# Optimization experiments

Hardware: AMD Instinct MI355X
Metric: run time of the kernel (lower is better)

The kernel has to match this reference:

```python
import jax, jax.numpy as jnp
import numpy as np

TGT, BSZ, E = 256, 8, 256
SRC = 4096
H = 8
HD = E // H


def setup_inputs() -> dict:
    key = jax.random.key(0)
    ks = jax.random.split(key, 6)
    return {
        "query": jax.random.normal(ks[0], (TGT, BSZ, E), dtype=jnp.float32),
        "key": jax.random.normal(ks[1], (SRC, BSZ, E), dtype=jnp.float32),
        "value": jax.random.normal(ks[2], (SRC, BSZ, E), dtype=jnp.float32),
        "proposal_mask": jax.random.uniform(ks[3], (BSZ, TGT, SRC), dtype=jnp.float32),
        "out_proj_weight": jax.random.normal(ks[4], (E, E), dtype=jnp.float32) * (1.0 / np.sqrt(E)),
        "out_proj_bias": jax.random.normal(ks[5], (E,), dtype=jnp.float32) * 0.01,
    }


def reference(query, key, value, proposal_mask, out_proj_weight, out_proj_bias):
    tgt_len, bsz, embed_dim = query.shape
    src_len = key.shape[0]
    num_heads = H
    head_dim = embed_dim // num_heads

    # v: (src, bsz, E) -> (src, bsz*H, hd) -> (bsz*H, src, hd); index q = b*H + h
    v = value.reshape(src_len, bsz * num_heads, head_dim).transpose(1, 0, 2)

    # proposal_mask (bsz, tgt, src); torch loop+stack produces mask_nhead[b*H+h] = proposal_mask[b]
    mask_nhead = jnp.repeat(proposal_mask, num_heads, axis=0)  # (bsz*H, tgt, src)

    # weighted sum of values per head (no score compute)
    attn_output = jnp.einsum('qts,qsc->qtc', mask_nhead, v)  # (bsz*H, tgt, hd)

    # (bsz*H, tgt, hd) -> (tgt, bsz*H, hd) -> (tgt, bsz, E)
    attn_output = attn_output.transpose(1, 0, 2).reshape(tgt_len, bsz, embed_dim)

    # out projection (outDecoderLayer=False)
    attn_output = attn_output @ out_proj_weight.T + out_proj_bias

    # averaged weights: mask repeated per head -> mean over heads == proposal_mask
    attn_weights = mask_nhead.reshape(bsz, num_heads, tgt_len, src_len).sum(axis=1) / num_heads
    return attn_output, attn_weights
```

## Files before the change

### kernel.cpp

```cpp
#include <hip/hip_runtime.h>
#include <hip/hip_bf16.h>

#define TGT 256
#define BSZ 8
#define E   256
#define SRC 4096

typedef __attribute__((ext_vector_type(8))) short           bf16x8;
typedef __attribute__((ext_vector_type(4))) float           f32x4;
typedef __attribute__((ext_vector_type(4))) float           f4;
typedef __attribute__((ext_vector_type(8))) unsigned short  u16x8;
typedef __attribute__((ext_vector_type(4))) unsigned short  u16x4;

__device__ inline unsigned short f2b(float x) {
    union { __hip_bfloat16 h; unsigned short u; } cv;
    cv.h = __float2bfloat16(x);
    return cv.u;
}

__device__ inline bf16x8 cvt8v(const float* __restrict__ p) {
    f4 lo = *(const f4*)p;
    f4 hi = *(const f4*)(p + 4);
    bf16x8 r;
    #pragma unroll
    for (int j = 0; j < 4; ++j) { r[j] = (short)f2b(lo[j]); r[4 + j] = (short)f2b(hi[j]); }
    return r;
}

__global__ __launch_bounds__(128) void prep_w(
    const float* __restrict__ wgt, unsigned short* __restrict__ wf)
{
    int o    = blockIdx.x * 128 + threadIdx.x;
    int et   = o >> 9;
    int ks   = (o >> 6) & 7;
    int lane = o & 63;
    int quad = lane >> 4, l15 = lane & 15;
    bf16x8 v = cvt8v(wgt + (size_t)(et * 16 + l15) * E + ks * 32 + quad * 8);
    *(bf16x8*)&wf[(size_t)o * 8] = v;
}

__global__ __launch_bounds__(512, 4) void prep_vw(
    const float* __restrict__ value, const unsigned short* __restrict__ wf,
    const float* __restrict__ bias,
    unsigned short* __restrict__ vwf, float* __restrict__ out0)
{
    const int tid = threadIdx.x;

    if (blockIdx.y == 8) {
        #pragma unroll
        for (int s = 0; s < 4; ++s) {
            int f4i = s * 32768 + blockIdx.x * 512 + tid;
            *(f4*)(out0 + (size_t)f4i * 4) = *(const f4*)(bias + (f4i & 63) * 4);
        }
        return;
    }

    __shared__ unsigned short tile[64 * 264];
    const int sc64 = blockIdx.x;
    const int b    = blockIdx.y;
    const int s0   = sc64 * 64;

    #pragma unroll
    for (int i = 0; i < 8; ++i) {
        int lin = i * 512 + tid;
        int row = lin >> 6;
        int c4  = lin & 63;
        f4 v = *(const f4*)(value + (size_t)(s0 + row) * (BSZ * E)
                                  + (size_t)b * E + c4 * 4);
        u16x4 pk;
        #pragma unroll
        for (int j = 0; j < 4; ++j) pk[j] = f2b(v[j]);
        *(u16x4*)&tile[row * 264 + c4 * 4] = pk;
    }
    __syncthreads();

    const int w    = tid >> 6;
    const int lane = tid & 63;
    const int quad = lane >> 4;
    const int l15  = lane & 15;
    const int mt   = w >> 1;
    const int et0  = (w & 1) * 8;

    bf16x8 a[8];
    #pragma unroll
    for (int ks = 0; ks < 8; ++ks)
        a[ks] = *(const bf16x8*)&tile[(mt * 16 + l15) * 264 + ks * 32 + quad * 8];
    __syncthreads();

    const unsigned short* bfw = wf + ((size_t)et0 * 8) * 512 + (size_t)lane * 8;
    f32x4 acc[8] = {};
    #pragma unroll
    for (int ks = 0; ks < 8; ++ks) {
        bf16x8 bb[8];
        #pragma unroll
        for (int e = 0; e < 8; ++e)
            bb[e] = *(const bf16x8*)(bfw + (size_t)(e * 8 + ks) * 512);
        #pragma unroll
        for (int e = 0; e < 8; ++e)
            acc[e] = __builtin_amdgcn_mfma_f32_16x16x32_bf16(a[ks], bb[e], acc[e], 0, 0, 0);
    }

    #pragma unroll
    for (int e = 0; e < 8; ++e)
        #pragma unroll
        for (int r = 0; r < 4; ++r)
            tile[(mt * 16 + quad * 4 + r) * 264 + (et0 + e) * 16 + l15] = f2b(acc[e][r]);
    __syncthreads();

    #pragma unroll
    for (int i = 0; i < 4; ++i) {
        int o    = i * 512 + tid;
        int et   = o >> 7;
        int ksl  = (o >> 6) & 1;
        int ln   = o & 63;
        int q2   = ln >> 4, p15 = ln & 15;
        u16x8 pk;
        #pragma unroll
        for (int j = 0; j < 8; ++j)
            pk[j] = tile[(ksl * 32 + q2 * 8 + j) * 264 + et * 16 + p15];
        size_t ks = (size_t)sc64 * 2 + ksl;
        *(u16x8*)&vwf[((((size_t)b * 16 + et) * 128 + ks) * 64 + ln) * 8] = pk;
    }
}

#define GP 520

__global__ __launch_bounds__(512, 4) void gemm1(
    const float* __restrict__ mask,
    const unsigned short* __restrict__ vwf,
    float* __restrict__ out1,
    float* __restrict__ out0)
{
    __shared__ unsigned short As[32 * GP];
    const int bx  = blockIdx.x;
    const int b   = bx & 7;
    const int tt  = (bx >> 3) & 7;
    const int kc  = bx >> 6;
    const int t0  = tt * 32;
    const int k0  = kc * 512;
    const int tid = threadIdx.x;
    const int w    = tid >> 6;
    const int lane = tid & 63;
    const int quad = lane >> 4;
    const int l15  = lane & 15;

    const float* mbase = mask + (size_t)b * TGT * SRC + (size_t)t0 * SRC + k0;
    float*       obase = out1 + (size_t)b * TGT * SRC + (size_t)t0 * SRC + k0;

    const int srow = tid >> 4;
    const int sc4  = tid & 15;
    f4 mv[8];
    #pragma unroll
    for (int j = 0; j < 8; ++j)
        mv[j] = *(const f4*)(mbase + (size_t)srow * SRC + (sc4 + j * 16) * 4);
    #pragma unroll
    for (int j = 0; j < 8; ++j) {
        u16x4 pk;
        #pragma unroll
        for (int t = 0; t < 4; ++t) pk[t] = f2b(mv[j][t]);
        *(u16x4*)&As[srow * GP + (sc4 + j * 16) * 4] = pk;
    }
    __syncthreads();

    #pragma unroll
    for (int j = 0; j < 8; ++j)
        *(f4*)(obase + (size_t)srow * SRC + (sc4 + j * 16) * 4) = mv[j];

    const unsigned short* bfr0 = vwf + (((size_t)b * 16 + 2 * w) * 128 + (size_t)kc * 16) * 512;
    const unsigned short* bfr1 = bfr0 + (size_t)128 * 512;

    f32x4 acc00 = {}, acc01 = {}, acc10 = {}, acc11 = {};
    #pragma unroll 4
    for (int q = 0; q < 16; ++q) {
        bf16x8 B0 = *(const bf16x8*)(bfr0 + ((size_t)q * 64 + lane) * 8);
        bf16x8 B1 = *(const bf16x8*)(bfr1 + ((size_t)q * 64 + lane) * 8);
        bf16x8 a0 = *(const bf16x8*)&As[ l15       * GP + q * 32 + quad * 8];
        bf16x8 a1 = *(const bf16x8*)&As[(l15 + 16) * GP + q * 32 + quad * 8];
        acc00 = __builtin_amdgcn_mfma_f32_16x16x32_bf16(a0, B0, acc00, 0, 0, 0);
        acc01 = __builtin_amdgcn_mfma_f32_16x16x32_bf16(a0, B1, acc01, 0, 0, 0);
        acc10 = __builtin_amdgcn_mfma_f32_16x16x32_bf16(a1, B0, acc10, 0, 0, 0);
        acc11 = __builtin_amdgcn_mfma_f32_16x16x32_bf16(a1, B1, acc11, 0, 0, 0);
    }

    {
        const int c0 = w * 32 + l15;
        #pragma unroll
        for (int r = 0; r < 4; ++r) {
            int tA = t0 + quad * 4 + r;
            int tB = tA + 16;
            float* oA = out0 + (size_t)tA * (BSZ * E) + (size_t)b * E;
            float* oB = out0 + (size_t)tB * (BSZ * E) + (size_t)b * E;
            atomicAdd(oA + c0,      acc00[r]);
            atomicAdd(oA + c0 + 16, acc01[r]);
            atomicAdd(oB + c0,      acc10[r]);
            atomicAdd(oB + c0 + 16, acc11[r]);
        }
    }
}

extern "C" void kernel_launch(void* const* d_in, const int* in_sizes, int n_in,
                              void* d_out, int out_size, void* d_ws, size_t ws_size,
                              hipStream_t stream)
{
    const float* value = (const float*)d_in[2];
    const float* mask  = (const float*)d_in[3];
    const float* wgt   = (const float*)d_in[4];
    const float* bias  = (const float*)d_in[5];

    float* out0 = (float*)d_out;
    float* out1 = (float*)d_out + (size_t)TGT * BSZ * E;

    unsigned short* vwf = (unsigned short*)d_ws;
    unsigned short* wf  = vwf + (size_t)BSZ * E * SRC;

    prep_w <<<64, 128, 0, stream>>>(wgt, wf);
    prep_vw<<<dim3(64, 9), 512, 0, stream>>>(value, wf, bias, vwf, out0);
    gemm1  <<<512, 512, 0, stream>>>(mask, vwf, out1, out0);
}
```

Measured before the change: 160.9 us.

## Halve tile sizes, write V·W fragments directly, use nontemporal mask streaming

Both prep_vw and gemm1 now run twice as many blocks of 256 threads over 32-row and 16-row tiles. prep_vw stores the MFMA accumulators straight into the B-fragment layout of vwf, which drops the shared-memory transpose stage and two barriers. gemm1 reads the mask and copies it to the weights output with nontemporal loads and stores so the streaming traffic does not pollute cache. Each gemm1 wave now computes four 16-column tiles against one A row block, so every vwf fragment is fetched by twice as many blocks.

```diff
diff --git a/kernel.cpp b/kernel.cpp
--- a/kernel.cpp
+++ b/kernel.cpp
@@ -39,7 +39,7 @@
     *(bf16x8*)&wf[(size_t)o * 8] = v;
 }
 
-__global__ __launch_bounds__(512, 4) void prep_vw(
+__global__ __launch_bounds__(256, 4) void prep_vw(
     const float* __restrict__ value, const unsigned short* __restrict__ wf,
     const float* __restrict__ bias,
     unsigned short* __restrict__ vwf, float* __restrict__ out0)
@@ -49,20 +49,20 @@
     if (blockIdx.y == 8) {
         #pragma unroll
         for (int s = 0; s < 4; ++s) {
-            int f4i = s * 32768 + blockIdx.x * 512 + tid;
+            int f4i = s * 32768 + blockIdx.x * 256 + tid;
             *(f4*)(out0 + (size_t)f4i * 4) = *(const f4*)(bias + (f4i & 63) * 4);
         }
         return;
     }
 
-    __shared__ unsigned short tile[64 * 264];
-    const int sc64 = blockIdx.x;
+    __shared__ unsigned short tile[32 * 264];
+    const int sc32 = blockIdx.x;
     const int b    = blockIdx.y;
-    const int s0   = sc64 * 64;
+    const int s0   = sc32 * 32;
 
     #pragma unroll
     for (int i = 0; i < 8; ++i) {
-        int lin = i * 512 + tid;
+        int lin = i * 256 + tid;
         int row = lin >> 6;
         int c4  = lin & 63;
         f4 v = *(const f4*)(value + (size_t)(s0 + row) * (BSZ * E)
@@ -85,7 +85,6 @@
     #pragma unroll
     for (int ks = 0; ks < 8; ++ks)
         a[ks] = *(const bf16x8*)&tile[(mt * 16 + l15) * 264 + ks * 32 + quad * 8];
-    __syncthreads();
 
     const unsigned short* bfw = wf + ((size_t)et0 * 8) * 512 + (size_t)lane * 8;
     f32x4 acc[8] = {};
@@ -100,43 +99,31 @@
             acc[e] = __builtin_amdgcn_mfma_f32_16x16x32_bf16(a[ks], bb[e], acc[e], 0, 0, 0);
     }
 
-    #pragma unroll
-    for (int e = 0; e < 8; ++e)
-        #pragma unroll
-        for (int r = 0; r < 4; ++r)
-            tile[(mt * 16 + quad * 4 + r) * 264 + (et0 + e) * 16 + l15] = f2b(acc[e][r]);
-    __syncthreads();
-
-    #pragma unroll
-    for (int i = 0; i < 4; ++i) {
-        int o    = i * 512 + tid;
-        int et   = o >> 7;
-        int ksl  = (o >> 6) & 1;
-        int ln   = o & 63;
-        int q2   = ln >> 4, p15 = ln & 15;
-        u16x8 pk;
-        #pragma unroll
-        for (int j = 0; j < 8; ++j)
-            pk[j] = tile[(ksl * 32 + q2 * 8 + j) * 264 + et * 16 + p15];
-        size_t ks = (size_t)sc64 * 2 + ksl;
-        *(u16x8*)&vwf[((((size_t)b * 16 + et) * 128 + ks) * 64 + ln) * 8] = pk;
+    const int lp = (mt * 2 + (quad >> 1)) * 16 + l15;
+    const int j0 = (quad & 1) * 4;
+    #pragma unroll
+    for (int e = 0; e < 8; ++e) {
+        u16x4 pk;
+        #pragma unroll
+        for (int r = 0; r < 4; ++r) pk[r] = f2b(acc[e][r]);
+        *(u16x4*)&vwf[((((size_t)b * 16 + et0 + e) * 128 + sc32) * 64 + lp) * 8 + j0] = pk;
     }
 }
 
 #define GP 520
 
-__global__ __launch_bounds__(512, 4) void gemm1(
+__global__ __launch_bounds__(256, 4) void gemm1(
     const float* __restrict__ mask,
     const unsigned short* __restrict__ vwf,
     float* __restrict__ out1,
     float* __restrict__ out0)
 {
-    __shared__ unsigned short As[32 * GP];
+    __shared__ unsigned short As[16 * GP];
     const int bx  = blockIdx.x;
     const int b   = bx & 7;
-    const int tt  = (bx >> 3) & 7;
-    const int kc  = bx >> 6;
-    const int t0  = tt * 32;
+    const int tt  = (bx >> 3) & 15;
+    const int kc  = bx >> 7;
+    const int t0  = tt * 16;
     const int k0  = kc * 512;
     const int tid = threadIdx.x;
     const int w    = tid >> 6;
@@ -152,7 +139,8 @@
     f4 mv[8];
     #pragma unroll
     for (int j = 0; j < 8; ++j)
-        mv[j] = *(const f4*)(mbase + (size_t)srow * SRC + (sc4 + j * 16) * 4);
+        mv[j] = __builtin_nontemporal_load(
+                    (const f4*)(mbase + (size_t)srow * SRC + (sc4 + j * 16) * 4));
     #pragma unroll
     for (int j = 0; j < 8; ++j) {
         u16x4 pk;
@@ -164,36 +152,33 @@
 
     #pragma unroll
     for (int j = 0; j < 8; ++j)
-        *(f4*)(obase + (size_t)srow * SRC + (sc4 + j * 16) * 4) = mv[j];
-
-    const unsigned short* bfr0 = vwf + (((size_t)b * 16 + 2 * w) * 128 + (size_t)kc * 16) * 512;
-    const unsigned short* bfr1 = bfr0 + (size_t)128 * 512;
-
-    f32x4 acc00 = {}, acc01 = {}, acc10 = {}, acc11 = {};
+        __builtin_nontemporal_store(
+            mv[j], (f4*)(obase + (size_t)srow * SRC + (sc4 + j * 16) * 4));
+
+    const unsigned short* bfr = vwf + (((size_t)b * 16 + (size_t)w * 4) * 128
+                                       + (size_t)kc * 16) * 512 + (size_t)lane * 8;
+
+    f32x4 acc[4] = {};
     #pragma unroll 4
     for (int q = 0; q < 16; ++q) {
-        bf16x8 B0 = *(const bf16x8*)(bfr0 + ((size_t)q * 64 + lane) * 8);
-        bf16x8 B1 = *(const bf16x8*)(bfr1 + ((size_t)q * 64 + lane) * 8);
-        bf16x8 a0 = *(const bf16x8*)&As[ l15       * GP + q * 32 + quad * 8];
-        bf16x8 a1 = *(const bf16x8*)&As[(l15 + 16) * GP + q * 32 + quad * 8];
-        acc00 = __builtin_amdgcn_mfma_f32_16x16x32_bf16(a0, B0, acc00, 0, 0, 0);
-        acc01 = __builtin_amdgcn_mfma_f32_16x16x32_bf16(a0, B1, acc01, 0, 0, 0);
-        acc10 = __builtin_amdgcn_mfma_f32_16x16x32_bf16(a1, B0, acc10, 0, 0, 0);
-        acc11 = __builtin_amdgcn_mfma_f32_16x16x32_bf16(a1, B1, acc11, 0, 0, 0);
-    }
-
-    {
-        const int c0 = w * 32 + l15;
+        bf16x8 a0 = *(const bf16x8*)&As[l15 * GP + q * 32 + quad * 8];
+        bf16x8 B0 = *(const bf16x8*)(bfr + ((size_t)0 * 128 + q) * 512);
+        bf16x8 B1 = *(const bf16x8*)(bfr + ((size_t)1 * 128 + q) * 512);
+        bf16x8 B2 = *(const bf16x8*)(bfr + ((size_t)2 * 128 + q) * 512);
+        bf16x8 B3 = *(const bf16x8*)(bfr + ((size_t)3 * 128 + q) * 512);
+        acc[0] = __builtin_amdgcn_mfma_f32_16x16x32_bf16(a0, B0, acc[0], 0, 0, 0);
+        acc[1] = __builtin_amdgcn_mfma_f32_16x16x32_bf16(a0, B1, acc[1], 0, 0, 0);
+        acc[2] = __builtin_amdgcn_mfma_f32_16x16x32_bf16(a0, B2, acc[2], 0, 0, 0);
+        acc[3] = __builtin_amdgcn_mfma_f32_16x16x32_bf16(a0, B3, acc[3], 0, 0, 0);
+    }
+
+    #pragma unroll
+    for (int e = 0; e < 4; ++e) {
+        int ecol = (w * 4 + e) * 16 + l15;
         #pragma unroll
         for (int r = 0; r < 4; ++r) {
-            int tA = t0 + quad * 4 + r;
-            int tB = tA + 16;
-            float* oA = out0 + (size_t)tA * (BSZ * E) + (size_t)b * E;
-            float* oB = out0 + (size_t)tB * (BSZ * E) + (size_t)b * E;
-            atomicAdd(oA + c0,      acc00[r]);
-            atomicAdd(oA + c0 + 16, acc01[r]);
-            atomicAdd(oB + c0,      acc10[r]);
-            atomicAdd(oB + c0 + 16, acc11[r]);
+            int t = t0 + quad * 4 + r;
+            atomicAdd(out0 + (size_t)t * (BSZ * E) + (size_t)b * E + ecol, acc[e][r]);
         }
     }
 }
@@ -214,6 +199,6 @@
     unsigned short* wf  = vwf + (size_t)BSZ * E * SRC;
 
     prep_w <<<64, 128, 0, stream>>>(wgt, wf);
-    prep_vw<<<dim3(64, 9), 512, 0, stream>>>(value, wf, bias, vwf, out0);
-    gemm1  <<<512, 512, 0, stream>>>(mask, vwf, out1, out0);
-}
+    prep_vw<<<dim3(128, 9), 256, 0, stream>>>(value, wf, bias, vwf, out0);
+    gemm1  <<<1024, 256, 0, stream>>>(mask, vwf, out1, out0);
+}
```

After: 164.7 us. +2.3%, slower.
